# Kernel tuning notes

Hardware: AMD Instinct MI355X
Metric: run time of the kernel (lower is better)

The kernel has to match this reference:

```python
import jax, jax.numpy as jnp
import numpy as np

N = 2000   # buses
E = 6000   # directed branches (each physical branch once)
T = 5
EPS = 1e-6
VM_MIN, VM_MAX = 0.5, 1.5


def setup_inputs() -> dict:
    key = jax.random.key(0)
    ks = jax.random.split(key, 16)
    va = 0.02 * jax.random.normal(ks[0], (N,), jnp.float32)
    vm = 1.0 + 0.02 * jax.random.normal(ks[1], (N,), jnp.float32)
    x = jnp.concatenate([va, vm])
    edge_index = jax.random.randint(ks[2], (2, E), 0, N)
    # physically plausible line parameters (avoid r=x=0 -> infinite admittance)
    br_r = 0.01 + 0.05 * jax.random.uniform(ks[3], (E,), jnp.float32)
    br_x = 0.02 + 0.10 * jax.random.uniform(ks[4], (E,), jnp.float32)
    g_fr = 0.01 * jax.random.uniform(ks[5], (E,), jnp.float32)
    b_fr = 0.01 * jax.random.uniform(ks[6], (E,), jnp.float32)
    g_to = 0.01 * jax.random.uniform(ks[7], (E,), jnp.float32)
    b_to = 0.01 * jax.random.uniform(ks[8], (E,), jnp.float32)
    tap = jnp.ones((E,), jnp.float32)
    shift = jnp.zeros((E,), jnp.float32)
    p_spec = 0.1 * jax.random.normal(ks[9], (N,), jnp.float32)
    q_spec = 0.1 * jax.random.normal(ks[10], (N,), jnp.float32)
    gs = 0.01 * jax.random.normal(ks[11], (N,), jnp.float32)
    bs = 0.01 * jax.random.normal(ks[12], (N,), jnp.float32)
    bus_type = jax.random.randint(ks[13], (N,), 1, 4)  # 1=PQ, 2=PV, 3=slack
    vm_setpoint = jnp.ones((N,), jnp.float32)
    return {"x": x, "edge_index": edge_index, "br_r": br_r, "br_x": br_x,
            "g_fr": g_fr, "b_fr": b_fr, "g_to": g_to, "b_to": b_to,
            "tap": tap, "shift": shift, "p_spec": p_spec, "q_spec": q_spec,
            "gs": gs, "bs": bs, "bus_type": bus_type, "vm_setpoint": vm_setpoint}


def _solve_unrolled(x, br_r, br_x, g_fr, b_fr, g_to, b_to, tap, shift,
                    p_spec, q_spec, gs, bs, vm_setpoint, edge_index, bus_type):
    n = x.shape[0] // 2
    dt = x.dtype
    src, dst = edge_index[0], edge_index[1]
    # series admittance y = 1/(r + jx), in real arithmetic
    denom = br_r * br_r + br_x * br_x
    g_s = br_r / denom
    b_s = -br_x / denom
    pv = bus_type == 2
    sl = bus_type == 3
    keep = jnp.concatenate([(~sl).astype(dt), (~(pv | sl)).astype(dt)])[:, None]
    override = jnp.concatenate([sl.astype(dt), (pv | sl).astype(dt)])
    rows = jnp.concatenate([src, src, dst, dst])
    cols = jnp.concatenate([src, dst, dst, src])

    def blk(vals):  # dense [n,n] block via scatter-add (COO)
        return jnp.zeros((n, n), dt).at[rows, cols].add(vals)

    cat = jnp.concatenate

    def step(x, _):
        va, vm = x[:n], x[n:]
        v_i, v_j = vm[src], vm[dst]
        th = va[src] - va[dst]
        cos_f = jnp.cos(th - shift); sin_f = jnp.sin(th - shift)
        cos_t = jnp.cos(shift - th); sin_t = jnp.sin(shift - th)
        vij_tau = v_i * v_j / tap
        # branch flows (pi-model)
        P_from = (v_i / tap) ** 2 * (g_s + g_fr) + vij_tau * (-g_s * cos_f - b_s * sin_f)
        Q_from = -(v_i / tap) ** 2 * (b_s + b_fr) + vij_tau * (-g_s * sin_f + b_s * cos_f)
        P_to = v_j ** 2 * (g_s + g_to) + vij_tau * (-g_s * cos_t - b_s * sin_t)
        Q_to = -v_j ** 2 * (b_s + b_to) + vij_tau * (-g_s * sin_t + b_s * cos_t)
        P_calc = jnp.zeros(n, dt).at[src].add(P_from).at[dst].add(P_to) + vm ** 2 * gs
        Q_calc = jnp.zeros(n, dt).at[src].add(Q_from).at[dst].add(Q_to) - vm ** 2 * bs
        # mismatch with bus-type overrides
        Fp = jnp.where(sl, va, p_spec - P_calc)
        Fq = jnp.where(pv | sl, vm - vm_setpoint, q_spec - Q_calc)
        F = jnp.concatenate([Fp, Fq])
        # analytical Jacobian entries
        A_f = g_s * cos_f + b_s * sin_f; B_f = g_s * sin_f - b_s * cos_f
        A_t = g_s * cos_t + b_s * sin_t; B_t = g_s * sin_t - b_s * cos_t
        dPfs_dth_src = vij_tau * B_f; dPfs_dth_dst = -vij_tau * B_f
        dPfs_dvm_src = 2.0 * v_i / tap ** 2 * (g_s + g_fr) - v_j / tap * A_f
        dPfs_dvm_dst = -(v_i / tap) * A_f
        dQfs_dth_src = -vij_tau * A_f; dQfs_dth_dst = vij_tau * A_f
        dQfs_dvm_src = -2.0 * v_i / tap ** 2 * (b_s + b_fr) - v_j / tap * B_f
        dQfs_dvm_dst = -(v_i / tap) * B_f
        dPfd_dth_dst = vij_tau * B_t; dPfd_dth_src = -vij_tau * B_t
        dPfd_dvm_dst = 2.0 * v_j * (g_s + g_to) - v_i / tap * A_t
        dPfd_dvm_src = -(v_j / tap) * A_t
        dQfd_dth_dst = -vij_tau * A_t; dQfd_dth_src = vij_tau * A_t
        dQfd_dvm_dst = -2.0 * v_j * (b_s + b_to) - v_i / tap * B_t
        dQfd_dvm_src = -(v_j / tap) * B_t
        dFP_dva = blk(cat([-dPfs_dth_src, -dPfs_dth_dst, -dPfd_dth_dst, -dPfd_dth_src]))
        dFP_dvm = blk(cat([-dPfs_dvm_src, -dPfs_dvm_dst, -dPfd_dvm_dst, -dPfd_dvm_src])) - jnp.diag(2.0 * vm * gs)
        dFQ_dva = blk(cat([-dQfs_dth_src, -dQfs_dth_dst, -dQfd_dth_dst, -dQfd_dth_src]))
        dFQ_dvm = blk(cat([-dQfs_dvm_src, -dQfs_dvm_dst, -dQfd_dvm_dst, -dQfd_dvm_src])) + jnp.diag(2.0 * vm * bs)
        J = jnp.block([[dFP_dva, dFP_dvm], [dFQ_dva, dFQ_dvm]])
        J = J * keep + jnp.diag(override)
        # Newton update with tiny Tikhonov regularization
        dx = jnp.linalg.solve(J + EPS * jnp.eye(2 * n, dtype=dt), F)
        x_new = x - dx
        vm_new = jnp.clip(x_new[n:], VM_MIN, VM_MAX)  # _project_voltage
        return jnp.concatenate([x_new[:n], vm_new]), None

    x_final, _ = jax.lax.scan(step, x, None, length=T)
    return x_final


def reference(x, edge_index, br_r, br_x, g_fr, b_fr, g_to, b_to, tap, shift,
              p_spec, q_spec, gs, bs, bus_type, vm_setpoint):
    return _solve_unrolled(x, br_r, br_x, g_fr, b_fr, g_to, b_to, tap, shift,
                           p_spec, q_spec, gs, bs, vm_setpoint, edge_index, bus_type)
```

## Files before the change

### kernel.cpp

```cpp
#include <hip/hip_runtime.h>
#include <math.h>

#define N_BUS 2000
#define N_EDGE 6000
#define N2 4000
#define NB 64
#define NPANELS 35
#define MPAD (NB * NPANELS)
#define LD 2308
#define DCOL 2244
#define T_STEPS 5
#define EPSR 1e-6f

__global__ __launch_bounds__(1024) void prep_once_kernel(
    const float* __restrict__ x, const int* __restrict__ bus_type,
    const float* __restrict__ br_r, const float* __restrict__ br_x,
    float* va, float* vm, float* gsa, float* bsa, int* kmap, int* m_dev) {
  __shared__ int cnt[1024];
  const int tid = threadIdx.x;
  int kept[4];
  int c = 0;
#pragma unroll
  for (int k = 0; k < 4; ++k) {
    int j = tid * 4 + k;
    kept[k] = 0;
    if (j < N2) {
      bool kp = (j < N_BUS) ? (bus_type[j] != 3) : (bus_type[j - N_BUS] == 1);
      kept[k] = kp ? 1 : 0;
      c += kept[k];
    }
  }
  cnt[tid] = c;
  __syncthreads();
  for (int off = 1; off < 1024; off <<= 1) {
    int v = cnt[tid];
    int u = (tid >= off) ? cnt[tid - off] : 0;
    __syncthreads();
    cnt[tid] = v + u;
    __syncthreads();
  }
  int base = cnt[tid] - c;
#pragma unroll
  for (int k = 0; k < 4; ++k) {
    int j = tid * 4 + k;
    if (j < N2) kmap[j] = kept[k] ? base++ : -1;
  }
  if (tid == 1023) *m_dev = cnt[1023];
  for (int e = tid; e < N_EDGE; e += 1024) {
    float r = br_r[e], xx = br_x[e];
    float den = r * r + xx * xx;
    gsa[e] = r / den;
    bsa[e] = -xx / den;
  }
  for (int i = tid; i < N_BUS; i += 1024) {
    va[i] = x[i];
    vm[i] = x[N_BUS + i];
  }
}

__global__ void step_prep_kernel(const int* __restrict__ bus_type,
                                 const float* __restrict__ vsp,
                                 const float* __restrict__ va,
                                 const float* __restrict__ vm,
                                 float* dxc, float* Pacc, float* Qacc) {
  int t = blockIdx.x * blockDim.x + threadIdx.x;
  if (t >= N2) return;
  if (t < N_BUS) {
    Pacc[t] = 0.f;
    Qacc[t] = 0.f;
    int bt = bus_type[t];
    dxc[t] = (bt == 3) ? va[t] / (1.f + EPSR) : 0.f;
  } else {
    int i = t - N_BUS;
    int bt = bus_type[i];
    dxc[t] = (bt >= 2) ? (vm[i] - vsp[i]) / (1.f + EPSR) : 0.f;
  }
}

__global__ void clear_M_kernel(float4* __restrict__ M4) {
  int t = blockIdx.x * blockDim.x + threadIdx.x;
  if (t < MPAD * LD / 4) M4[t] = float4{0.f, 0.f, 0.f, 0.f};
}

__device__ __forceinline__ void addJ(float* __restrict__ M,
                                     const int* __restrict__ kmap,
                                     const float* __restrict__ dxc, int r,
                                     int C, float v) {
  int c = kmap[C];
  if (c >= 0)
    atomicAdd(&M[(size_t)r * LD + c], v);
  else
    atomicAdd(&M[(size_t)r * LD + MPAD], -v * dxc[C]);
}

__global__ void edge_kernel(const int* __restrict__ ei,
                            const float* __restrict__ gsa,
                            const float* __restrict__ bsa,
                            const float* __restrict__ g_fr,
                            const float* __restrict__ b_fr,
                            const float* __restrict__ g_to,
                            const float* __restrict__ b_to,
                            const float* __restrict__ tapA,
                            const float* __restrict__ shiftA,
                            const float* __restrict__ va,
                            const float* __restrict__ vm,
                            const int* __restrict__ kmap,
                            const float* __restrict__ dxc,
                            float* __restrict__ M, float* __restrict__ Pacc,
                            float* __restrict__ Qacc) {
  int e = blockIdx.x * blockDim.x + threadIdx.x;
  if (e >= N_EDGE) return;
  int s = ei[e], d = ei[N_EDGE + e];
  float g = gsa[e], b = bsa[e];
  float ti = 1.f / tapA[e];
  float vi = vm[s], vj = vm[d];
  float th = (va[s] - va[d]) - shiftA[e];
  float cf = cosf(th), sf = sinf(th);
  float vij = vi * vj * ti;
  float Af = g * cf + b * sf, Bf = g * sf - b * cf;
  float At = g * cf - b * sf, Bt = -g * sf - b * cf;
  float vit = vi * ti;
  float Pf = vit * vit * (g + g_fr[e]) + vij * (-g * cf - b * sf);
  float Qf = -vit * vit * (b + b_fr[e]) + vij * (-g * sf + b * cf);
  float Pt = vj * vj * (g + g_to[e]) + vij * (-g * cf + b * sf);
  float Qt = -vj * vj * (b + b_to[e]) + vij * (g * sf + b * cf);
  atomicAdd(&Pacc[s], Pf);
  atomicAdd(&Qacc[s], Qf);
  atomicAdd(&Pacc[d], Pt);
  atomicAdd(&Qacc[d], Qt);
  int rPs = kmap[s], rPd = kmap[d];
  int rQs = kmap[N_BUS + s], rQd = kmap[N_BUS + d];
  if (rPs >= 0) {
    addJ(M, kmap, dxc, rPs, s, -vij * Bf);
    addJ(M, kmap, dxc, rPs, d, vij * Bf);
    addJ(M, kmap, dxc, rPs, N_BUS + s,
         -2.f * vi * ti * ti * (g + g_fr[e]) + vj * ti * Af);
    addJ(M, kmap, dxc, rPs, N_BUS + d, vi * ti * Af);
  }
  if (rQs >= 0) {
    addJ(M, kmap, dxc, rQs, s, vij * Af);
    addJ(M, kmap, dxc, rQs, d, -vij * Af);
    addJ(M, kmap, dxc, rQs, N_BUS + s,
         2.f * vi * ti * ti * (b + b_fr[e]) + vj * ti * Bf);
    addJ(M, kmap, dxc, rQs, N_BUS + d, vi * ti * Bf);
  }
  if (rPd >= 0) {
    addJ(M, kmap, dxc, rPd, d, -vij * Bt);
    addJ(M, kmap, dxc, rPd, s, vij * Bt);
    addJ(M, kmap, dxc, rPd, N_BUS + d,
         -2.f * vj * (g + g_to[e]) + vi * ti * At);
    addJ(M, kmap, dxc, rPd, N_BUS + s, vj * ti * At);
  }
  if (rQd >= 0) {
    addJ(M, kmap, dxc, rQd, d, vij * At);
    addJ(M, kmap, dxc, rQd, s, -vij * At);
    addJ(M, kmap, dxc, rQd, N_BUS + d,
         2.f * vj * (b + b_to[e]) + vi * ti * Bt);
    addJ(M, kmap, dxc, rQd, N_BUS + s, vj * ti * Bt);
  }
}

__global__ void finalize_kernel(const float* __restrict__ p_spec,
                                const float* __restrict__ q_spec,
                                const float* __restrict__ gsN,
                                const float* __restrict__ bsN,
                                const float* __restrict__ va,
                                const float* __restrict__ vm,
                                const int* __restrict__ kmap,
                                const float* __restrict__ dxc,
                                const int* __restrict__ m_dev,
                                float* __restrict__ M,
                                const float* __restrict__ Pacc,
                                const float* __restrict__ Qacc) {
  int t = blockIdx.x * blockDim.x + threadIdx.x;
  if (t < N_BUS) {
    int r = kmap[t];
    if (r >= 0) {
      float* row = &M[(size_t)r * LD];
      row[r] += EPSR;
      int cq = kmap[N_BUS + t];
      float val = -2.f * vm[t] * gsN[t];
      if (cq >= 0)
        row[cq] += val;
      else
        row[MPAD] -= val * dxc[N_BUS + t];
      float Pc = Pacc[t] + vm[t] * vm[t] * gsN[t];
      row[MPAD] += p_spec[t] - Pc;
    }
  } else if (t < N2) {
    int i = t - N_BUS;
    int r = kmap[t];
    if (r >= 0) {
      float* row = &M[(size_t)r * LD];
      row[r] += 2.f * vm[i] * bsN[i] + EPSR;
      float Qc = Qacc[i] - vm[i] * vm[i] * bsN[i];
      row[MPAD] += q_spec[i] - Qc;
    }
  } else if (t < N2 + MPAD) {
    int r = t - N2;
    if (r >= *m_dev) M[(size_t)r * LD + r] = 1.f;
  }
}

__device__ __forceinline__ void lu64_nopivot(float (*A)[68], int tid) {
#pragma unroll 1
  for (int k = 0; k < 63; ++k) {
    float dinv = 1.f / A[k][k];
    if (tid > k && tid < 64) A[tid][k] *= dinv;
    __syncthreads();
    int c = tid & 63, q = tid >> 6;
    if (c > k) {
      float ukc = A[k][c];
      for (int r = k + 1 + q; r < 64; r += 4)
        A[r][c] = fmaf(-A[r][k], ukc, A[r][c]);
    }
    __syncthreads();
  }
}

__global__ __launch_bounds__(256) void factor0_kernel(float* __restrict__ M) {
  __shared__ __align__(16) float A[64][68];
  const int tid = threadIdx.x;
  for (int idx = tid; idx < 64 * 16; idx += 256) {
    int i = idx >> 4, j4 = idx & 15;
    *(float4*)&A[i][j4 * 4] = *(const float4*)&M[(size_t)i * LD + j4 * 4];
  }
  __syncthreads();
  lu64_nopivot(A, tid);
  for (int idx = tid; idx < 64 * 64; idx += 256)
    M[(size_t)(idx >> 6) * LD + DCOL + (idx & 63)] = A[idx >> 6][idx & 63];
}

__global__ __launch_bounds__(64) void trsm_kernel(float* __restrict__ M,
                                                  int pan, int ncb) {
  const int s0 = pan * NB, s1 = s0 + NB;
  const int tid = threadIdx.x;
  __shared__ __align__(16) float Ls[64][68];
  __shared__ float sDi[64];
  for (int k = 0; k < 16; ++k) {
    int idx = tid + 64 * k;
    int i = idx >> 4, j4 = idx & 15;
    *(float4*)&Ls[i][j4 * 4] =
        *(const float4*)&M[(size_t)(s0 + i) * LD + DCOL + j4 * 4];
  }
  __syncthreads();
  sDi[tid] = 1.f / Ls[tid][tid];
  __syncthreads();

  if (blockIdx.x < ncb) {
    int cc = s1 + blockIdx.x * 64 + tid;
    if (cc <= MPAD) {
      float y[64];
#pragma unroll
      for (int i = 0; i < 64; ++i) y[i] = M[(size_t)(s0 + i) * LD + cc];
#pragma unroll
      for (int i4 = 0; i4 < 16; ++i4) {
        const int i0 = i4 * 4;
        float a0 = y[i0], a1 = y[i0 + 1], a2 = y[i0 + 2], a3 = y[i0 + 3];
#pragma unroll
        for (int j4 = 0; j4 < i4; ++j4) {
          const int j0 = j4 * 4;
          float yj0 = y[j0], yj1 = y[j0 + 1], yj2 = y[j0 + 2], yj3 = y[j0 + 3];
          float4 l0 = *(const float4*)&Ls[i0 + 0][j0];
          float4 l1 = *(const float4*)&Ls[i0 + 1][j0];
          float4 l2 = *(const float4*)&Ls[i0 + 2][j0];
          float4 l3 = *(const float4*)&Ls[i0 + 3][j0];
          a0 = fmaf(-l0.x, yj0, fmaf(-l0.y, yj1, fmaf(-l0.z, yj2, fmaf(-l0.w, yj3, a0))));
          a1 = fmaf(-l1.x, yj0, fmaf(-l1.y, yj1, fmaf(-l1.z, yj2, fmaf(-l1.w, yj3, a1))));
          a2 = fmaf(-l2.x, yj0, fmaf(-l2.y, yj1, fmaf(-l2.z, yj2, fmaf(-l2.w, yj3, a2))));
          a3 = fmaf(-l3.x, yj0, fmaf(-l3.y, yj1, fmaf(-l3.z, yj2, fmaf(-l3.w, yj3, a3))));
        }
        a1 = fmaf(-Ls[i0 + 1][i0], a0, a1);
        a2 = fmaf(-Ls[i0 + 2][i0], a0, fmaf(-Ls[i0 + 2][i0 + 1], a1, a2));
        a3 = fmaf(-Ls[i0 + 3][i0], a0,
                  fmaf(-Ls[i0 + 3][i0 + 1], a1, fmaf(-Ls[i0 + 3][i0 + 2], a2, a3)));
        y[i0] = a0; y[i0 + 1] = a1; y[i0 + 2] = a2; y[i0 + 3] = a3;
      }
#pragma unroll
      for (int i = 0; i < 64; ++i) M[(size_t)(s0 + i) * LD + cc] = y[i];
    }
  } else {
    int r = s1 + (blockIdx.x - ncb) * 64 + tid;
    if (r < MPAD) {
      float a[64];
#pragma unroll
      for (int j4 = 0; j4 < 16; ++j4) {
        float4 t = *(const float4*)&M[(size_t)r * LD + s0 + j4 * 4];
        a[j4 * 4] = t.x; a[j4 * 4 + 1] = t.y;
        a[j4 * 4 + 2] = t.z; a[j4 * 4 + 3] = t.w;
      }
#pragma unroll
      for (int j4 = 0; j4 < 16; ++j4) {
        const int j0 = j4 * 4;
        float b0_ = a[j0], b1 = a[j0 + 1], b2 = a[j0 + 2], b3 = a[j0 + 3];
#pragma unroll
        for (int k4 = 0; k4 < j4; ++k4) {
#pragma unroll
          for (int dk = 0; dk < 4; ++dk) {
            float xk = a[k4 * 4 + dk];
            float4 u = *(const float4*)&Ls[k4 * 4 + dk][j0];
            b0_ = fmaf(-xk, u.x, b0_);
            b1 = fmaf(-xk, u.y, b1);
            b2 = fmaf(-xk, u.z, b2);
            b3 = fmaf(-xk, u.w, b3);
          }
        }
        b0_ *= sDi[j0];
        b1 = fmaf(-b0_, Ls[j0][j0 + 1], b1) * sDi[j0 + 1];
        b2 = fmaf(-b0_, Ls[j0][j0 + 2], fmaf(-b1, Ls[j0 + 1][j0 + 2], b2)) *
             sDi[j0 + 2];
        b3 = fmaf(-b0_, Ls[j0][j0 + 3],
                  fmaf(-b1, Ls[j0 + 1][j0 + 3],
                       fmaf(-b2, Ls[j0 + 2][j0 + 3], b3))) *
             sDi[j0 + 3];
        a[j0] = b0_; a[j0 + 1] = b1; a[j0 + 2] = b2; a[j0 + 3] = b3;
      }
#pragma unroll
      for (int j4 = 0; j4 < 16; ++j4) {
        float4 t{a[j4 * 4], a[j4 * 4 + 1], a[j4 * 4 + 2], a[j4 * 4 + 3]};
        *(float4*)&M[(size_t)r * LD + s0 + j4 * 4] = t;
      }
    }
  }
}

__global__ __launch_bounds__(256) void gemm_kernel(float* __restrict__ M,
                                                   int pan) {
  const int s0 = pan * NB, s1 = s0 + NB;
  const int r0 = s1 + blockIdx.x * 64;
  const int c0 = s1 + blockIdx.y * 64;
  __shared__ __align__(16) float As[64][68];
  __shared__ __align__(16) float Bs[64][68];
  const int tid = threadIdx.x;
  for (int idx = tid; idx < 64 * 16; idx += 256) {
    int i = idx >> 4, j4 = idx & 15;
    *(float4*)&As[i][j4 * 4] =
        *(const float4*)&M[(size_t)(r0 + i) * LD + s0 + j4 * 4];
    *(float4*)&Bs[i][j4 * 4] =
        *(const float4*)&M[(size_t)(s0 + i) * LD + c0 + j4 * 4];
  }
  __syncthreads();
  const int tr = (tid >> 4) * 4;
  const int tc = (tid & 15) * 4;
  float acc[4][4] = {};
#pragma unroll
  for (int k4 = 0; k4 < 16; ++k4) {
    float ar[4][4], br[4][4];
#pragma unroll
    for (int i = 0; i < 4; ++i) {
      float4 t = *(const float4*)&As[tr + i][k4 * 4];
      ar[i][0] = t.x; ar[i][1] = t.y; ar[i][2] = t.z; ar[i][3] = t.w;
    }
#pragma unroll
    for (int kk = 0; kk < 4; ++kk) {
      float4 t = *(const float4*)&Bs[k4 * 4 + kk][tc];
      br[kk][0] = t.x; br[kk][1] = t.y; br[kk][2] = t.z; br[kk][3] = t.w;
    }
#pragma unroll
    for (int kk = 0; kk < 4; ++kk)
#pragma unroll
      for (int i = 0; i < 4; ++i)
#pragma unroll
        for (int jj = 0; jj < 4; ++jj)
          acc[i][jj] = fmaf(ar[i][kk], br[kk][jj], acc[i][jj]);
  }
  __syncthreads();
  const bool fb = (blockIdx.x == 0 && blockIdx.y == 0);
  const bool lastc = (c0 == MPAD);
#pragma unroll
  for (int i = 0; i < 4; ++i) {
    float* crow = &M[(size_t)(r0 + tr + i) * LD + c0 + tc];
    float4 cv = *(float4*)crow;
    cv.x -= acc[i][0];
    cv.y -= acc[i][1];
    cv.z -= acc[i][2];
    cv.w -= acc[i][3];
    if (!lastc) {
      *(float4*)crow = cv;
    } else {
      if (c0 + tc + 0 <= MPAD) crow[0] = cv.x;
      if (c0 + tc + 1 <= MPAD) crow[1] = cv.y;
      if (c0 + tc + 2 <= MPAD) crow[2] = cv.z;
      if (c0 + tc + 3 <= MPAD) crow[3] = cv.w;
    }
    if (fb) {
      As[tr + i][tc + 0] = cv.x;
      As[tr + i][tc + 1] = cv.y;
      As[tr + i][tc + 2] = cv.z;
      As[tr + i][tc + 3] = cv.w;
    }
  }
  if (fb) {
    __syncthreads();
    lu64_nopivot(As, tid);
    for (int idx = tid; idx < 64 * 64; idx += 256)
      M[(size_t)(s1 + (idx >> 6)) * LD + DCOL + (idx & 63)] =
          As[idx >> 6][idx & 63];
  }
}

__global__ __launch_bounds__(1024) void backsub_kernel(
    const float* __restrict__ M, float* __restrict__ dx) {
  __shared__ float ys[MPAD];
  __shared__ __align__(16) float Ds[64][68];
  __shared__ float sDi[64];
  const int tid = threadIdx.x;
  for (int r = tid; r < MPAD; r += 1024) ys[r] = M[(size_t)r * LD + MPAD];
  __syncthreads();
  for (int jb = NPANELS - 1; jb >= 0; --jb) {
    const int b0 = jb * NB;
    for (int idx = tid; idx < 64 * 16; idx += 1024) {
      int i = idx >> 4, j4 = idx & 15;
      *(float4*)&Ds[i][j4 * 4] =
          *(const float4*)&M[(size_t)(b0 + i) * LD + DCOL + j4 * 4];
    }
    __syncthreads();
    if (tid < 64) sDi[tid] = 1.f / Ds[tid][tid];
    __syncthreads();
    if (tid < 64) {
      for (int i = 63; i >= 0; --i) {
        float xv = ys[b0 + i] * sDi[i];
        if (tid == i) ys[b0 + i] = xv;
        if (tid < i) ys[b0 + tid] = fmaf(-Ds[tid][i], xv, ys[b0 + tid]);
      }
    }
    __syncthreads();
    if (b0 > 0) {
      const int q = tid & 15;
      float4 xq = *(const float4*)&ys[b0 + q * 4];
      for (int r = (tid >> 4); r < b0; r += 64) {
        float4 u = *(const float4*)&M[(size_t)r * LD + b0 + q * 4];
        float p = u.x * xq.x + u.y * xq.y + u.z * xq.z + u.w * xq.w;
        p += __shfl_down(p, 8, 16);
        p += __shfl_down(p, 4, 16);
        p += __shfl_down(p, 2, 16);
        p += __shfl_down(p, 1, 16);
        if (q == 0) ys[r] -= p;
      }
    }
    __syncthreads();
  }
  for (int r = tid; r < MPAD; r += 1024) dx[r] = ys[r];
}

__global__ void update_kernel(const int* __restrict__ kmap,
                              const float* __restrict__ dx,
                              const float* __restrict__ dxc, float* va,
                              float* vm, float* __restrict__ out) {
  int t = blockIdx.x * blockDim.x + threadIdx.x;
  if (t >= N2) return;
  int r = kmap[t];
  float d = (r >= 0) ? dx[r] : dxc[t];
  if (t < N_BUS) {
    float v = va[t] - d;
    va[t] = v;
    out[t] = v;
  } else {
    int i = t - N_BUS;
    float v = vm[i] - d;
    v = fminf(fmaxf(v, 0.5f), 1.5f);
    vm[i] = v;
    out[t] = v;
  }
}

extern "C" void kernel_launch(void* const* d_in, const int* in_sizes, int n_in,
                              void* d_out, int out_size, void* d_ws,
                              size_t ws_size, hipStream_t stream) {
  const float* x = (const float*)d_in[0];
  const int* ei = (const int*)d_in[1];
  const float* br_r = (const float*)d_in[2];
  const float* br_x = (const float*)d_in[3];
  const float* g_fr = (const float*)d_in[4];
  const float* b_fr = (const float*)d_in[5];
  const float* g_to = (const float*)d_in[6];
  const float* b_to = (const float*)d_in[7];
  const float* tap = (const float*)d_in[8];
  const float* shift = (const float*)d_in[9];
  const float* p_spec = (const float*)d_in[10];
  const float* q_spec = (const float*)d_in[11];
  const float* gsN = (const float*)d_in[12];
  const float* bsN = (const float*)d_in[13];
  const int* bus_type = (const int*)d_in[14];
  const float* vsp = (const float*)d_in[15];
  float* out = (float*)d_out;

  float* W = (float*)d_ws;
  float* M = W;
  float* dx = W + (size_t)MPAD * LD;
  float* dxc = dx + MPAD;
  float* va = dxc + N2;
  float* vm = va + N_BUS;
  float* Pacc = vm + N_BUS;
  float* Qacc = Pacc + N_BUS;
  float* gsa = Qacc + N_BUS;
  float* bsa = gsa + N_EDGE;
  int* kmap = (int*)(bsa + N_EDGE);
  int* m_dev = kmap + N2;

  prep_once_kernel<<<1, 1024, 0, stream>>>(x, bus_type, br_r, br_x, va, vm,
                                           gsa, bsa, kmap, m_dev);
  for (int t = 0; t < T_STEPS; ++t) {
    step_prep_kernel<<<(N2 + 255) / 256, 256, 0, stream>>>(bus_type, vsp, va,
                                                           vm, dxc, Pacc, Qacc);
    clear_M_kernel<<<(MPAD * LD / 4 + 255) / 256, 256, 0, stream>>>(
        (float4*)M);
    edge_kernel<<<(N_EDGE + 255) / 256, 256, 0, stream>>>(
        ei, gsa, bsa, g_fr, b_fr, g_to, b_to, tap, shift, va, vm, kmap, dxc, M,
        Pacc, Qacc);
    finalize_kernel<<<(N2 + MPAD + 255) / 256, 256, 0, stream>>>(
        p_spec, q_spec, gsN, bsN, va, vm, kmap, dxc, m_dev, M, Pacc, Qacc);
    factor0_kernel<<<1, 256, 0, stream>>>(M);
    for (int p = 0; p < NPANELS; ++p) {
      int s1 = (p + 1) * NB;
      int w = MPAD - s1 + 1;
      int ncb = (w + 63) / 64;
      int nrb = (MPAD - s1 + 63) / 64;
      trsm_kernel<<<ncb + nrb, 64, 0, stream>>>(M, p, ncb);
      int tr_ = NPANELS - 1 - p;
      int tc_ = NPANELS - p;
      if (tr_ > 0) {
        dim3 g(tr_, tc_);
        gemm_kernel<<<g, 256, 0, stream>>>(M, p);
      }
    }
    backsub_kernel<<<1, 1024, 0, stream>>>(M, dx);
    update_kernel<<<(N2 + 255) / 256, 256, 0, stream>>>(kmap, dx, dxc, va, vm,
                                                        out);
  }
}
```

Measured before the change: 14.72 ms.

## Replace blocked LU trsm+gemm with inverted-diagonal-block Schur updates

```diff
diff --git a/kernel.cpp b/kernel.cpp
--- a/kernel.cpp
+++ b/kernel.cpp
@@ -58,28 +58,26 @@
   }
 }
 
-__global__ void step_prep_kernel(const int* __restrict__ bus_type,
-                                 const float* __restrict__ vsp,
-                                 const float* __restrict__ va,
-                                 const float* __restrict__ vm,
-                                 float* dxc, float* Pacc, float* Qacc) {
-  int t = blockIdx.x * blockDim.x + threadIdx.x;
-  if (t >= N2) return;
-  if (t < N_BUS) {
-    Pacc[t] = 0.f;
-    Qacc[t] = 0.f;
-    int bt = bus_type[t];
-    dxc[t] = (bt == 3) ? va[t] / (1.f + EPSR) : 0.f;
-  } else {
-    int i = t - N_BUS;
-    int bt = bus_type[i];
-    dxc[t] = (bt >= 2) ? (vm[i] - vsp[i]) / (1.f + EPSR) : 0.f;
-  }
-}
-
-__global__ void clear_M_kernel(float4* __restrict__ M4) {
+__global__ void clear_prep_kernel(float4* __restrict__ M4,
+                                  const int* __restrict__ bus_type,
+                                  const float* __restrict__ vsp,
+                                  const float* __restrict__ va,
+                                  const float* __restrict__ vm, float* dxc,
+                                  float* Pacc, float* Qacc) {
   int t = blockIdx.x * blockDim.x + threadIdx.x;
   if (t < MPAD * LD / 4) M4[t] = float4{0.f, 0.f, 0.f, 0.f};
+  if (t < N2) {
+    if (t < N_BUS) {
+      Pacc[t] = 0.f;
+      Qacc[t] = 0.f;
+      int bt = bus_type[t];
+      dxc[t] = (bt == 3) ? va[t] / (1.f + EPSR) : 0.f;
+    } else {
+      int i = t - N_BUS;
+      int bt = bus_type[i];
+      dxc[t] = (bt >= 2) ? (vm[i] - vsp[i]) / (1.f + EPSR) : 0.f;
+    }
+  }
 }
 
 __device__ __forceinline__ void addJ(float* __restrict__ M,
@@ -202,232 +200,215 @@
   }
 }
 
-__device__ __forceinline__ void lu64_nopivot(float (*A)[68], int tid) {
+__device__ __forceinline__ void gj_invert64(float (*A)[68],
+                                            float* __restrict__ colk,
+                                            int tid) {
 #pragma unroll 1
-  for (int k = 0; k < 63; ++k) {
-    float dinv = 1.f / A[k][k];
-    if (tid > k && tid < 64) A[tid][k] *= dinv;
-    __syncthreads();
-    int c = tid & 63, q = tid >> 6;
-    if (c > k) {
-      float ukc = A[k][c];
-      for (int r = k + 1 + q; r < 64; r += 4)
-        A[r][c] = fmaf(-A[r][k], ukc, A[r][c]);
-    }
-    __syncthreads();
-  }
-}
-
-__global__ __launch_bounds__(256) void factor0_kernel(float* __restrict__ M) {
+  for (int k = 0; k < 64; ++k) {
+    if (tid < 64) colk[tid] = A[tid][k];
+    __syncthreads();
+    float d = 1.f / colk[k];
+    if (tid < 64) A[k][tid] = (tid == k) ? d : A[k][tid] * d;
+    __syncthreads();
+    int c = tid & 63;
+    float rkc = A[k][c];
+    for (int i = (tid >> 6); i < 64; i += 4) {
+      if (i != k) {
+        float e = colk[i];
+        A[i][c] = (c == k) ? (-e * d) : fmaf(-e, rkc, A[i][c]);
+      }
+    }
+    __syncthreads();
+  }
+}
+
+__global__ __launch_bounds__(256) void invert0_kernel(float* __restrict__ M) {
   __shared__ __align__(16) float A[64][68];
+  __shared__ float colk[64];
   const int tid = threadIdx.x;
   for (int idx = tid; idx < 64 * 16; idx += 256) {
-    int i = idx >> 4, j4 = idx & 15;
-    *(float4*)&A[i][j4 * 4] = *(const float4*)&M[(size_t)i * LD + j4 * 4];
+    int r = idx >> 4, q = idx & 15;
+    *(float4*)&A[r][q * 4] = *(const float4*)&M[(size_t)r * LD + q * 4];
   }
   __syncthreads();
-  lu64_nopivot(A, tid);
+  gj_invert64(A, colk, tid);
   for (int idx = tid; idx < 64 * 64; idx += 256)
     M[(size_t)(idx >> 6) * LD + DCOL + (idx & 63)] = A[idx >> 6][idx & 63];
 }
 
-__global__ __launch_bounds__(64) void trsm_kernel(float* __restrict__ M,
-                                                  int pan, int ncb) {
+__global__ __launch_bounds__(256) void schur_kernel(float* __restrict__ M,
+                                                    int pan) {
   const int s0 = pan * NB, s1 = s0 + NB;
+  const int tcr = NPANELS - 1 - pan;
+  const int i = blockIdx.x + 1;
+  const int j = blockIdx.y + 1;
+  const int r0 = s0 + i * 64;
   const int tid = threadIdx.x;
-  __shared__ __align__(16) float Ls[64][68];
-  __shared__ float sDi[64];
-  for (int k = 0; k < 16; ++k) {
-    int idx = tid + 64 * k;
-    int i = idx >> 4, j4 = idx & 15;
-    *(float4*)&Ls[i][j4 * 4] =
-        *(const float4*)&M[(size_t)(s0 + i) * LD + DCOL + j4 * 4];
-  }
-  __syncthreads();
-  sDi[tid] = 1.f / Ls[tid][tid];
-  __syncthreads();
-
-  if (blockIdx.x < ncb) {
-    int cc = s1 + blockIdx.x * 64 + tid;
-    if (cc <= MPAD) {
-      float y[64];
-#pragma unroll
-      for (int i = 0; i < 64; ++i) y[i] = M[(size_t)(s0 + i) * LD + cc];
-#pragma unroll
-      for (int i4 = 0; i4 < 16; ++i4) {
-        const int i0 = i4 * 4;
-        float a0 = y[i0], a1 = y[i0 + 1], a2 = y[i0 + 2], a3 = y[i0 + 3];
-#pragma unroll
-        for (int j4 = 0; j4 < i4; ++j4) {
-          const int j0 = j4 * 4;
-          float yj0 = y[j0], yj1 = y[j0 + 1], yj2 = y[j0 + 2], yj3 = y[j0 + 3];
-          float4 l0 = *(const float4*)&Ls[i0 + 0][j0];
-          float4 l1 = *(const float4*)&Ls[i0 + 1][j0];
-          float4 l2 = *(const float4*)&Ls[i0 + 2][j0];
-          float4 l3 = *(const float4*)&Ls[i0 + 3][j0];
-          a0 = fmaf(-l0.x, yj0, fmaf(-l0.y, yj1, fmaf(-l0.z, yj2, fmaf(-l0.w, yj3, a0))));
-          a1 = fmaf(-l1.x, yj0, fmaf(-l1.y, yj1, fmaf(-l1.z, yj2, fmaf(-l1.w, yj3, a1))));
-          a2 = fmaf(-l2.x, yj0, fmaf(-l2.y, yj1, fmaf(-l2.z, yj2, fmaf(-l2.w, yj3, a2))));
-          a3 = fmaf(-l3.x, yj0, fmaf(-l3.y, yj1, fmaf(-l3.z, yj2, fmaf(-l3.w, yj3, a3))));
-        }
-        a1 = fmaf(-Ls[i0 + 1][i0], a0, a1);
-        a2 = fmaf(-Ls[i0 + 2][i0], a0, fmaf(-Ls[i0 + 2][i0 + 1], a1, a2));
-        a3 = fmaf(-Ls[i0 + 3][i0], a0,
-                  fmaf(-Ls[i0 + 3][i0 + 1], a1, fmaf(-Ls[i0 + 3][i0 + 2], a2, a3)));
-        y[i0] = a0; y[i0 + 1] = a1; y[i0 + 2] = a2; y[i0 + 3] = a3;
-      }
-#pragma unroll
-      for (int i = 0; i < 64; ++i) M[(size_t)(s0 + i) * LD + cc] = y[i];
+  __shared__ __align__(16) float Gs[64][68];
+  __shared__ __align__(16) float Bs[64][68];
+  __shared__ __align__(16) float As[64][68];
+  __shared__ float colk[64];
+  __shared__ float zf[64];
+
+  for (int idx = tid; idx < 64 * 16; idx += 256) {
+    int r = idx >> 4, q = idx & 15;
+    *(float4*)&Gs[r][q * 4] =
+        *(const float4*)&M[(size_t)(s0 + r) * LD + DCOL + q * 4];
+  }
+
+  if (j <= tcr) {
+    const int c0 = s0 + j * 64;
+    for (int idx = tid; idx < 64 * 16; idx += 256) {
+      int r = idx >> 4, q = idx & 15;
+      *(float4*)&Bs[r][q * 4] =
+          *(const float4*)&M[(size_t)(s0 + r) * LD + c0 + q * 4];
+      *(float4*)&As[r][q * 4] =
+          *(const float4*)&M[(size_t)(r0 + r) * LD + s0 + q * 4];
+    }
+    __syncthreads();
+    const int tr = (tid >> 4) * 4;
+    const int tc = (tid & 15) * 4;
+    float accB[4][4] = {};
+#pragma unroll
+    for (int k4 = 0; k4 < 16; ++k4) {
+      float ar[4][4], br[4][4];
+#pragma unroll
+      for (int ii = 0; ii < 4; ++ii) {
+        float4 t = *(const float4*)&Gs[tr + ii][k4 * 4];
+        ar[ii][0] = t.x; ar[ii][1] = t.y; ar[ii][2] = t.z; ar[ii][3] = t.w;
+      }
+#pragma unroll
+      for (int kk = 0; kk < 4; ++kk) {
+        float4 t = *(const float4*)&Bs[k4 * 4 + kk][tc];
+        br[kk][0] = t.x; br[kk][1] = t.y; br[kk][2] = t.z; br[kk][3] = t.w;
+      }
+#pragma unroll
+      for (int kk = 0; kk < 4; ++kk)
+#pragma unroll
+        for (int ii = 0; ii < 4; ++ii)
+#pragma unroll
+          for (int jj = 0; jj < 4; ++jj)
+            accB[ii][jj] = fmaf(ar[ii][kk], br[kk][jj], accB[ii][jj]);
+    }
+    __syncthreads();
+#pragma unroll
+    for (int ii = 0; ii < 4; ++ii) {
+      float4 t{accB[ii][0], accB[ii][1], accB[ii][2], accB[ii][3]};
+      *(float4*)&Bs[tr + ii][tc] = t;
+    }
+    __syncthreads();
+    float accC[4][4] = {};
+#pragma unroll
+    for (int k4 = 0; k4 < 16; ++k4) {
+      float ar[4][4], br[4][4];
+#pragma unroll
+      for (int ii = 0; ii < 4; ++ii) {
+        float4 t = *(const float4*)&As[tr + ii][k4 * 4];
+        ar[ii][0] = t.x; ar[ii][1] = t.y; ar[ii][2] = t.z; ar[ii][3] = t.w;
+      }
+#pragma unroll
+      for (int kk = 0; kk < 4; ++kk) {
+        float4 t = *(const float4*)&Bs[k4 * 4 + kk][tc];
+        br[kk][0] = t.x; br[kk][1] = t.y; br[kk][2] = t.z; br[kk][3] = t.w;
+      }
+#pragma unroll
+      for (int kk = 0; kk < 4; ++kk)
+#pragma unroll
+        for (int ii = 0; ii < 4; ++ii)
+#pragma unroll
+          for (int jj = 0; jj < 4; ++jj)
+            accC[ii][jj] = fmaf(ar[ii][kk], br[kk][jj], accC[ii][jj]);
+    }
+    float cnew[4][4];
+#pragma unroll
+    for (int ii = 0; ii < 4; ++ii) {
+      float* crow = &M[(size_t)(r0 + tr + ii) * LD + c0 + tc];
+      float4 cv = *(float4*)crow;
+      cv.x -= accC[ii][0];
+      cv.y -= accC[ii][1];
+      cv.z -= accC[ii][2];
+      cv.w -= accC[ii][3];
+      *(float4*)crow = cv;
+      cnew[ii][0] = cv.x; cnew[ii][1] = cv.y;
+      cnew[ii][2] = cv.z; cnew[ii][3] = cv.w;
+    }
+    if (i == 1 && j == 1) {
+      __syncthreads();
+#pragma unroll
+      for (int ii = 0; ii < 4; ++ii) {
+        float4 t{cnew[ii][0], cnew[ii][1], cnew[ii][2], cnew[ii][3]};
+        *(float4*)&Gs[tr + ii][tc] = t;
+      }
+      __syncthreads();
+      gj_invert64(Gs, colk, tid);
+      for (int idx = tid; idx < 64 * 64; idx += 256)
+        M[(size_t)(s1 + (idx >> 6)) * LD + DCOL + (idx & 63)] =
+            Gs[idx >> 6][idx & 63];
     }
   } else {
-    int r = s1 + (blockIdx.x - ncb) * 64 + tid;
-    if (r < MPAD) {
-      float a[64];
-#pragma unroll
-      for (int j4 = 0; j4 < 16; ++j4) {
-        float4 t = *(const float4*)&M[(size_t)r * LD + s0 + j4 * 4];
-        a[j4 * 4] = t.x; a[j4 * 4 + 1] = t.y;
-        a[j4 * 4 + 2] = t.z; a[j4 * 4 + 3] = t.w;
-      }
-#pragma unroll
-      for (int j4 = 0; j4 < 16; ++j4) {
-        const int j0 = j4 * 4;
-        float b0_ = a[j0], b1 = a[j0 + 1], b2 = a[j0 + 2], b3 = a[j0 + 3];
-#pragma unroll
-        for (int k4 = 0; k4 < j4; ++k4) {
-#pragma unroll
-          for (int dk = 0; dk < 4; ++dk) {
-            float xk = a[k4 * 4 + dk];
-            float4 u = *(const float4*)&Ls[k4 * 4 + dk][j0];
-            b0_ = fmaf(-xk, u.x, b0_);
-            b1 = fmaf(-xk, u.y, b1);
-            b2 = fmaf(-xk, u.z, b2);
-            b3 = fmaf(-xk, u.w, b3);
-          }
-        }
-        b0_ *= sDi[j0];
-        b1 = fmaf(-b0_, Ls[j0][j0 + 1], b1) * sDi[j0 + 1];
-        b2 = fmaf(-b0_, Ls[j0][j0 + 2], fmaf(-b1, Ls[j0 + 1][j0 + 2], b2)) *
-             sDi[j0 + 2];
-        b3 = fmaf(-b0_, Ls[j0][j0 + 3],
-                  fmaf(-b1, Ls[j0 + 1][j0 + 3],
-                       fmaf(-b2, Ls[j0 + 2][j0 + 3], b3))) *
-             sDi[j0 + 3];
-        a[j0] = b0_; a[j0 + 1] = b1; a[j0 + 2] = b2; a[j0 + 3] = b3;
-      }
-#pragma unroll
-      for (int j4 = 0; j4 < 16; ++j4) {
-        float4 t{a[j4 * 4], a[j4 * 4 + 1], a[j4 * 4 + 2], a[j4 * 4 + 3]};
-        *(float4*)&M[(size_t)r * LD + s0 + j4 * 4] = t;
-      }
-    }
-  }
-}
-
-__global__ __launch_bounds__(256) void gemm_kernel(float* __restrict__ M,
-                                                   int pan) {
-  const int s0 = pan * NB, s1 = s0 + NB;
-  const int r0 = s1 + blockIdx.x * 64;
-  const int c0 = s1 + blockIdx.y * 64;
-  __shared__ __align__(16) float As[64][68];
-  __shared__ __align__(16) float Bs[64][68];
-  const int tid = threadIdx.x;
-  for (int idx = tid; idx < 64 * 16; idx += 256) {
-    int i = idx >> 4, j4 = idx & 15;
-    *(float4*)&As[i][j4 * 4] =
-        *(const float4*)&M[(size_t)(r0 + i) * LD + s0 + j4 * 4];
-    *(float4*)&Bs[i][j4 * 4] =
-        *(const float4*)&M[(size_t)(s0 + i) * LD + c0 + j4 * 4];
-  }
-  __syncthreads();
-  const int tr = (tid >> 4) * 4;
-  const int tc = (tid & 15) * 4;
-  float acc[4][4] = {};
-#pragma unroll
-  for (int k4 = 0; k4 < 16; ++k4) {
-    float ar[4][4], br[4][4];
-#pragma unroll
-    for (int i = 0; i < 4; ++i) {
-      float4 t = *(const float4*)&As[tr + i][k4 * 4];
-      ar[i][0] = t.x; ar[i][1] = t.y; ar[i][2] = t.z; ar[i][3] = t.w;
-    }
-#pragma unroll
-    for (int kk = 0; kk < 4; ++kk) {
-      float4 t = *(const float4*)&Bs[k4 * 4 + kk][tc];
-      br[kk][0] = t.x; br[kk][1] = t.y; br[kk][2] = t.z; br[kk][3] = t.w;
-    }
-#pragma unroll
-    for (int kk = 0; kk < 4; ++kk)
-#pragma unroll
-      for (int i = 0; i < 4; ++i)
-#pragma unroll
-        for (int jj = 0; jj < 4; ++jj)
-          acc[i][jj] = fmaf(ar[i][kk], br[kk][jj], acc[i][jj]);
-  }
-  __syncthreads();
-  const bool fb = (blockIdx.x == 0 && blockIdx.y == 0);
-  const bool lastc = (c0 == MPAD);
-#pragma unroll
-  for (int i = 0; i < 4; ++i) {
-    float* crow = &M[(size_t)(r0 + tr + i) * LD + c0 + tc];
-    float4 cv = *(float4*)crow;
-    cv.x -= acc[i][0];
-    cv.y -= acc[i][1];
-    cv.z -= acc[i][2];
-    cv.w -= acc[i][3];
-    if (!lastc) {
-      *(float4*)crow = cv;
-    } else {
-      if (c0 + tc + 0 <= MPAD) crow[0] = cv.x;
-      if (c0 + tc + 1 <= MPAD) crow[1] = cv.y;
-      if (c0 + tc + 2 <= MPAD) crow[2] = cv.z;
-      if (c0 + tc + 3 <= MPAD) crow[3] = cv.w;
-    }
-    if (fb) {
-      As[tr + i][tc + 0] = cv.x;
-      As[tr + i][tc + 1] = cv.y;
-      As[tr + i][tc + 2] = cv.z;
-      As[tr + i][tc + 3] = cv.w;
-    }
-  }
-  if (fb) {
-    __syncthreads();
-    lu64_nopivot(As, tid);
-    for (int idx = tid; idx < 64 * 64; idx += 256)
-      M[(size_t)(s1 + (idx >> 6)) * LD + DCOL + (idx & 63)] =
-          As[idx >> 6][idx & 63];
+    if (tid < 64) colk[tid] = M[(size_t)(s0 + tid) * LD + MPAD];
+    __syncthreads();
+    if (tid < 64) {
+      float z = 0.f;
+#pragma unroll
+      for (int k4 = 0; k4 < 16; ++k4) {
+        float4 g = *(const float4*)&Gs[tid][k4 * 4];
+        z = fmaf(g.x, colk[k4 * 4 + 0],
+            fmaf(g.y, colk[k4 * 4 + 1],
+            fmaf(g.z, colk[k4 * 4 + 2], fmaf(g.w, colk[k4 * 4 + 3], z))));
+      }
+      zf[tid] = z;
+    }
+    __syncthreads();
+    if (tid < 64) {
+      float acc = 0.f;
+#pragma unroll
+      for (int k4 = 0; k4 < 16; ++k4) {
+        float4 a = *(const float4*)&M[(size_t)(r0 + tid) * LD + s0 + k4 * 4];
+        acc = fmaf(a.x, zf[k4 * 4 + 0],
+              fmaf(a.y, zf[k4 * 4 + 1],
+              fmaf(a.z, zf[k4 * 4 + 2], fmaf(a.w, zf[k4 * 4 + 3], acc))));
+      }
+      size_t off = (size_t)(r0 + tid) * LD + MPAD;
+      M[off] = M[off] - acc;
+    }
   }
 }
 
 __global__ __launch_bounds__(1024) void backsub_kernel(
-    const float* __restrict__ M, float* __restrict__ dx) {
+    const float* __restrict__ M, const int* __restrict__ kmap,
+    const float* __restrict__ dxc, float* va, float* vm,
+    float* __restrict__ out) {
   __shared__ float ys[MPAD];
-  __shared__ __align__(16) float Ds[64][68];
-  __shared__ float sDi[64];
+  __shared__ __align__(16) float Gs[64][68];
+  __shared__ float xs[64];
   const int tid = threadIdx.x;
   for (int r = tid; r < MPAD; r += 1024) ys[r] = M[(size_t)r * LD + MPAD];
   __syncthreads();
   for (int jb = NPANELS - 1; jb >= 0; --jb) {
     const int b0 = jb * NB;
-    for (int idx = tid; idx < 64 * 16; idx += 1024) {
-      int i = idx >> 4, j4 = idx & 15;
-      *(float4*)&Ds[i][j4 * 4] =
-          *(const float4*)&M[(size_t)(b0 + i) * LD + DCOL + j4 * 4];
-    }
-    __syncthreads();
-    if (tid < 64) sDi[tid] = 1.f / Ds[tid][tid];
-    __syncthreads();
-    if (tid < 64) {
-      for (int i = 63; i >= 0; --i) {
-        float xv = ys[b0 + i] * sDi[i];
-        if (tid == i) ys[b0 + i] = xv;
-        if (tid < i) ys[b0 + tid] = fmaf(-Ds[tid][i], xv, ys[b0 + tid]);
-      }
-    }
-    __syncthreads();
+    {
+      int r = tid >> 4, q = tid & 15;
+      *(float4*)&Gs[r][q * 4] =
+          *(const float4*)&M[(size_t)(b0 + r) * LD + DCOL + q * 4];
+    }
+    __syncthreads();
+    {
+      int r = tid >> 4, q = tid & 15;
+      float4 g = *(const float4*)&Gs[r][q * 4];
+      float p = g.x * ys[b0 + q * 4] + g.y * ys[b0 + q * 4 + 1] +
+                g.z * ys[b0 + q * 4 + 2] + g.w * ys[b0 + q * 4 + 3];
+      p += __shfl_down(p, 8, 16);
+      p += __shfl_down(p, 4, 16);
+      p += __shfl_down(p, 2, 16);
+      p += __shfl_down(p, 1, 16);
+      if (q == 0) xs[r] = p;
+    }
+    __syncthreads();
+    if (tid < 64) ys[b0 + tid] = xs[tid];
     if (b0 > 0) {
       const int q = tid & 15;
-      float4 xq = *(const float4*)&ys[b0 + q * 4];
+      float4 xq = *(const float4*)&xs[q * 4];
       for (int r = (tid >> 4); r < b0; r += 64) {
         float4 u = *(const float4*)&M[(size_t)r * LD + b0 + q * 4];
         float p = u.x * xq.x + u.y * xq.y + u.z * xq.z + u.w * xq.w;
@@ -440,27 +421,20 @@
     }
     __syncthreads();
   }
-  for (int r = tid; r < MPAD; r += 1024) dx[r] = ys[r];
-}
-
-__global__ void update_kernel(const int* __restrict__ kmap,
-                              const float* __restrict__ dx,
-                              const float* __restrict__ dxc, float* va,
-                              float* vm, float* __restrict__ out) {
-  int t = blockIdx.x * blockDim.x + threadIdx.x;
-  if (t >= N2) return;
-  int r = kmap[t];
-  float d = (r >= 0) ? dx[r] : dxc[t];
-  if (t < N_BUS) {
-    float v = va[t] - d;
-    va[t] = v;
-    out[t] = v;
-  } else {
-    int i = t - N_BUS;
-    float v = vm[i] - d;
-    v = fminf(fmaxf(v, 0.5f), 1.5f);
-    vm[i] = v;
-    out[t] = v;
+  for (int t = tid; t < N2; t += 1024) {
+    int r = kmap[t];
+    float d = (r >= 0) ? ys[r] : dxc[t];
+    if (t < N_BUS) {
+      float v = va[t] - d;
+      va[t] = v;
+      out[t] = v;
+    } else {
+      int i2 = t - N_BUS;
+      float v = vm[i2] - d;
+      v = fminf(fmaxf(v, 0.5f), 1.5f);
+      vm[i2] = v;
+      out[t] = v;
+    }
   }
 }
 
@@ -487,8 +461,7 @@
 
   float* W = (float*)d_ws;
   float* M = W;
-  float* dx = W + (size_t)MPAD * LD;
-  float* dxc = dx + MPAD;
+  float* dxc = W + (size_t)MPAD * LD;
   float* va = dxc + N2;
   float* vm = va + N_BUS;
   float* Pacc = vm + N_BUS;
@@ -500,32 +473,21 @@
 
   prep_once_kernel<<<1, 1024, 0, stream>>>(x, bus_type, br_r, br_x, va, vm,
                                            gsa, bsa, kmap, m_dev);
+  const int clear_blocks = (MPAD * LD / 4 + 255) / 256;
   for (int t = 0; t < T_STEPS; ++t) {
-    step_prep_kernel<<<(N2 + 255) / 256, 256, 0, stream>>>(bus_type, vsp, va,
-                                                           vm, dxc, Pacc, Qacc);
-    clear_M_kernel<<<(MPAD * LD / 4 + 255) / 256, 256, 0, stream>>>(
-        (float4*)M);
+    clear_prep_kernel<<<clear_blocks, 256, 0, stream>>>(
+        (float4*)M, bus_type, vsp, va, vm, dxc, Pacc, Qacc);
     edge_kernel<<<(N_EDGE + 255) / 256, 256, 0, stream>>>(
         ei, gsa, bsa, g_fr, b_fr, g_to, b_to, tap, shift, va, vm, kmap, dxc, M,
         Pacc, Qacc);
     finalize_kernel<<<(N2 + MPAD + 255) / 256, 256, 0, stream>>>(
         p_spec, q_spec, gsN, bsN, va, vm, kmap, dxc, m_dev, M, Pacc, Qacc);
-    factor0_kernel<<<1, 256, 0, stream>>>(M);
-    for (int p = 0; p < NPANELS; ++p) {
-      int s1 = (p + 1) * NB;
-      int w = MPAD - s1 + 1;
-      int ncb = (w + 63) / 64;
-      int nrb = (MPAD - s1 + 63) / 64;
-      trsm_kernel<<<ncb + nrb, 64, 0, stream>>>(M, p, ncb);
+    invert0_kernel<<<1, 256, 0, stream>>>(M);
+    for (int p = 0; p < NPANELS - 1; ++p) {
       int tr_ = NPANELS - 1 - p;
-      int tc_ = NPANELS - p;
-      if (tr_ > 0) {
-        dim3 g(tr_, tc_);
-        gemm_kernel<<<g, 256, 0, stream>>>(M, p);
-      }
-    }
-    backsub_kernel<<<1, 1024, 0, stream>>>(M, dx);
-    update_kernel<<<(N2 + 255) / 256, 256, 0, stream>>>(kmap, dx, dxc, va, vm,
-                                                        out);
-  }
-}
+      dim3 g(tr_, tr_ + 1);
+      schur_kernel<<<g, 256, 0, stream>>>(M, p);
+    }
+    backsub_kernel<<<1, 1024, 0, stream>>>(M, kmap, dxc, va, vm, out);
+  }
+}
```

Measured after the change: 25.01 ms. +70.0%, slower.
